# Optimization experiments

Measured on AMD Instinct MI355X. Metric: run time of the kernel, lower is better.

The kernel has to match this reference:

```python
import jax, jax.numpy as jnp
import numpy as np

B, D = 32768, 256          # batch, latent_size
L, K = 4, 2048             # n_codebooks, codebook_size
BETA = 0.25                # commitment loss weight (EMA layer uses only beta term)


def setup_inputs() -> dict:
    key = jax.random.key(0)
    kx, kc = jax.random.split(key)
    x = jax.random.normal(kx, (B, D), dtype=jnp.float32)
    # per-level codebooks (EMAVQLayer.embed, xavier-normal-ish scale)
    codebooks = jax.random.normal(kc, (L, K, D), dtype=jnp.float32) * 0.1
    return {"x": x, "codebooks": codebooks}


def reference(x, codebooks):
    """RQLayer.forward (EMA variant, eval-path math; EMA buffer updates are
    side effects and do not change forward outputs)."""
    sg = jax.lax.stop_gradient
    quantized = jnp.zeros_like(x)
    loss = jnp.zeros((), x.dtype)
    unused = jnp.zeros((), jnp.int32)
    inds = []
    for l in range(L):  # small fixed number of residual levels
        c = codebooks[l]                                   # [K, D]
        dist = (jnp.sum(x * x, axis=1, keepdims=True)
                - 2.0 * (x @ c.T)
                + jnp.sum(c * c, axis=1)[None, :])
        ind = jnp.argmin(dist, axis=1)                     # [B]
        x_q = c[ind]                                       # gather [B, D]
        counts = jnp.zeros((K,), jnp.int32).at[ind].add(1)
        unused = unused + jnp.sum(counts == 0)
        loss = loss + BETA * jnp.mean((x - sg(x_q)) ** 2)
        quant = x + sg(x_q - x)                            # straight-through
        x = x - quant                                      # residual (== sg(x - x_q))
        quantized = quantized + quant
        inds.append(ind)
    return quantized, loss / L, unused, jnp.stack(inds, axis=1)
```

## Files before the change

### kernel.cpp

```cpp
#include <hip/hip_runtime.h>

#define NT 512
#define B_ 32768
#define D_ 256
#define L_ 4
#define K_ 2048
#define BM 64
#define NBLK (B_/BM)
#define BETA_ 0.25f

#define OUT_LOSS   8388608
#define OUT_UNUSED 8388609
#define OUT_INDS   8388610


__global__ __launch_bounds__(256) void rq_prep(const float* __restrict__ cb,
                                               int* __restrict__ counts,
                                               float* __restrict__ cnorm) {
  int cw = blockIdx.x * 256 + threadIdx.x;
  if (cw >= L_ * K_) return;
  counts[cw] = 0;
  const float4* cb4 = (const float4*)cb;
  float s = 0.f;
  for (int d4 = 0; d4 < 64; ++d4) {
    float4 v = cb4[(size_t)cw * 64 + d4];
    s = __fadd_rn(s, __fmul_rn(v.x, v.x));
    s = __fadd_rn(s, __fmul_rn(v.y, v.y));
    s = __fadd_rn(s, __fmul_rn(v.z, v.z));
    s = __fadd_rn(s, __fmul_rn(v.w, v.w));
  }
  cnorm[cw] = s;
}

template<int CTRL>
__device__ __forceinline__ float dpp_f(float v) {
  return __int_as_float(__builtin_amdgcn_update_dpp(0, __float_as_int(v), CTRL, 0xF, 0xF, true));
}
template<int CTRL>
__device__ __forceinline__ int dpp_i(int v) {
  return __builtin_amdgcn_update_dpp(0, v, CTRL, 0xF, 0xF, true);
}
#define XOR1 0xB1
#define XOR2 0x4E

__global__ __attribute__((amdgpu_flat_work_group_size(NT, NT), amdgpu_waves_per_eu(1)))
void rq_main(
    const float* __restrict__ x, const float* __restrict__ cb,
    float* __restrict__ out, int* __restrict__ counts,
    const float* __restrict__ cnorm, float* __restrict__ lpart) {
  __shared__ float4 xs[64][65];
  __shared__ float4 cs[64][64];
  __shared__ float  red_v[8][64];
  __shared__ int    red_i[8][64];
  __shared__ float  xxs[64];
  __shared__ int    ind_s[64];
  __shared__ float  lred[NT];

  const int tid  = threadIdx.x;
  const int lane = tid & 63;
  const int wave = tid >> 6;
  const int dg   = lane & 3;
  const int p    = lane >> 2;
  const int row0 = blockIdx.x * BM;
  const float4* x4  = (const float4*)x;
  const float4* cb4 = (const float4*)cb;

  {
    float4 v[8];
    #pragma unroll
    for (int it = 0; it < 8; ++it)
      v[it] = x4[(size_t)(row0 + wave + (it << 3)) * 64 + lane];
    #pragma unroll
    for (int it = 0; it < 8; ++it)
      xs[wave + (it << 3)][lane] = v[it];
  }

  float4 st[8];
  #pragma unroll
  for (int it = 0; it < 8; ++it)
    st[it] = cb4[(size_t)(wave * 8 + it) * 64 + lane];
  #pragma unroll
  for (int it = 0; it < 8; ++it)
    cs[wave * 8 + it][lane] = st[it];

  const float4* xb = &xs[p * 4][dg];
  const float4* cvp[4];
  #pragma unroll
  for (int jj = 0; jj < 4; ++jj) cvp[jj] = &cs[wave * 8 + (jj ^ dg)][dg];

  float lsum = 0.f;
  const int kb = (wave << 3) | dg;
  float4* out4 = (float4*)out;

  for (int l = 0; l < L_; ++l) {
    __syncthreads();

    if (tid < 64) {
      float s = 0.f;
      for (int d4 = 0; d4 < 64; ++d4) {
        float4 v = xs[tid][d4];
        s = __fadd_rn(s, __fmul_rn(v.x, v.x));
        s = __fadd_rn(s, __fmul_rn(v.y, v.y));
        s = __fadd_rn(s, __fmul_rn(v.z, v.z));
        s = __fadd_rn(s, __fmul_rn(v.w, v.w));
      }
      xxs[tid] = s;
    }
    __syncthreads();

    float xxr[4];
    #pragma unroll
    for (int i = 0; i < 4; ++i) xxr[i] = xxs[p * 4 + i];

    float bv[4]; int bi[4];
    #pragma unroll
    for (int i = 0; i < 4; ++i) { bv[i] = 3.4e38f; bi[i] = 0; }
    const float* cnl = cnorm + l * K_;

    for (int ch = 0; ch < 32; ++ch) {
      {
        int tn = l * 32 + ch + 1; if (tn > 127) tn = 127;
        const float4* src = cb4 + (size_t)tn * 4096;
        #pragma unroll
        for (int it = 0; it < 8; ++it)
          st[it] = src[(size_t)(wave * 8 + it) * 64 + lane];
      }
      const float cn0 = cnl[(ch << 6) + kb];
      const float cn4 = cnl[(ch << 6) + kb + 4];

      float acc[4][8];

      {
        float4 xv[4], cv[8];
        #pragma unroll
        for (int i = 0; i < 4; ++i) xv[i] = xb[i * 65];
        #pragma unroll
        for (int j = 0; j < 4; ++j) { cv[j] = cvp[j][0]; cv[j + 4] = cvp[j][256]; }
        #pragma unroll
        for (int i = 0; i < 4; ++i)
          #pragma unroll
          for (int j = 0; j < 8; ++j) {
            float a = __fmul_rn(xv[i].x, cv[j].x);
            a = fmaf(xv[i].y, cv[j].y, a);
            a = fmaf(xv[i].z, cv[j].z, a);
            a = fmaf(xv[i].w, cv[j].w, a);
            acc[i][j] = a;
          }
      }
      #pragma unroll
      for (int t = 1; t < 16; ++t) {
        float4 xv[4], cv[8];
        #pragma unroll
        for (int i = 0; i < 4; ++i) xv[i] = xb[i * 65 + t * 4];
        #pragma unroll
        for (int j = 0; j < 4; ++j) { cv[j] = cvp[j][t * 4]; cv[j + 4] = cvp[j][t * 4 + 256]; }
        #pragma unroll
        for (int i = 0; i < 4; ++i)
          #pragma unroll
          for (int j = 0; j < 8; ++j) {
            acc[i][j] = fmaf(xv[i].x, cv[j].x, acc[i][j]);
            acc[i][j] = fmaf(xv[i].y, cv[j].y, acc[i][j]);
            acc[i][j] = fmaf(xv[i].z, cv[j].z, acc[i][j]);
            acc[i][j] = fmaf(xv[i].w, cv[j].w, acc[i][j]);
          }
      }

      #pragma unroll
      for (int it = 0; it < 8; ++it)
        cs[wave * 8 + it][lane] = st[it];

      #pragma unroll
      for (int i = 0; i < 4; ++i) {
        acc[i][0] += dpp_f<XOR1>(acc[i][1]);
        acc[i][2] += dpp_f<XOR1>(acc[i][3]);
        acc[i][0] += dpp_f<XOR2>(acc[i][2]);
        acc[i][4] += dpp_f<XOR1>(acc[i][5]);
        acc[i][6] += dpp_f<XOR1>(acc[i][7]);
        acc[i][4] += dpp_f<XOR2>(acc[i][6]);
      }

      const int kidx = (ch << 6) + kb;
      #pragma unroll
      for (int i = 0; i < 4; ++i) {
        float s0 = __fadd_rn(__fsub_rn(xxr[i], __fmul_rn(2.0f, acc[i][0])), cn0);
        if (s0 < bv[i]) { bv[i] = s0; bi[i] = kidx; }
        float s4 = __fadd_rn(__fsub_rn(xxr[i], __fmul_rn(2.0f, acc[i][4])), cn4);
        if (s4 < bv[i]) { bv[i] = s4; bi[i] = kidx + 4; }
      }
    }

    #pragma unroll
    for (int i = 0; i < 4; ++i) {
      { float pv = dpp_f<XOR1>(bv[i]); int pi = dpp_i<XOR1>(bi[i]);
        if (pv < bv[i] || (pv == bv[i] && pi < bi[i])) { bv[i] = pv; bi[i] = pi; } }
      { float pv = dpp_f<XOR2>(bv[i]); int pi = dpp_i<XOR2>(bi[i]);
        if (pv < bv[i] || (pv == bv[i] && pi < bi[i])) { bv[i] = pv; bi[i] = pi; } }
    }
    if (dg == 0) {
      #pragma unroll
      for (int i = 0; i < 4; ++i) {
        red_v[wave][p * 4 + i] = bv[i];
        red_i[wave][p * 4 + i] = bi[i];
      }
    }
    __syncthreads();
    if (tid < 64) {
      float bv_ = red_v[0][tid]; int bi_ = red_i[0][tid];
      #pragma unroll
      for (int w = 1; w < 8; ++w) {
        float v = red_v[w][tid]; int ii = red_i[w][tid];
        if (v < bv_ || (v == bv_ && ii < bi_)) { bv_ = v; bi_ = ii; }
      }
      ind_s[tid] = bi_;
      out[(size_t)OUT_INDS + (size_t)(row0 + tid) * L_ + l] = (float)bi_;
      atomicAdd(&counts[l * K_ + bi_], 1);
    }
    __syncthreads();

    #pragma unroll
    for (int it = 0; it < 8; ++it) {
      const int r = wave + (it << 3);
      const size_t oidx = (size_t)(row0 + r) * 64 + lane;
      float4 xv = xs[r][lane];
      float4 cv = cb4[(size_t)(l * K_ + ind_s[r]) * 64 + lane];
      float tx = __fsub_rn(cv.x, xv.x); float qx = __fadd_rn(xv.x, tx); float nx = __fsub_rn(xv.x, qx);
      float ty = __fsub_rn(cv.y, xv.y); float qy = __fadd_rn(xv.y, ty); float ny = __fsub_rn(xv.y, qy);
      float tz = __fsub_rn(cv.z, xv.z); float qz = __fadd_rn(xv.z, tz); float nz = __fsub_rn(xv.z, qz);
      float tw = __fsub_rn(cv.w, xv.w); float qw = __fadd_rn(xv.w, tw); float nw = __fsub_rn(xv.w, qw);
      float4 prev = (l == 0) ? make_float4(0.f, 0.f, 0.f, 0.f) : out4[oidx];
      out4[oidx] = make_float4(__fadd_rn(prev.x, qx), __fadd_rn(prev.y, qy),
                               __fadd_rn(prev.z, qz), __fadd_rn(prev.w, qw));
      float ex = __fsub_rn(xv.x, cv.x);
      float ey = __fsub_rn(xv.y, cv.y);
      float ez = __fsub_rn(xv.z, cv.z);
      float ew = __fsub_rn(xv.w, cv.w);
      lsum = __fadd_rn(lsum, __fmul_rn(ex, ex));
      lsum = __fadd_rn(lsum, __fmul_rn(ey, ey));
      lsum = __fadd_rn(lsum, __fmul_rn(ez, ez));
      lsum = __fadd_rn(lsum, __fmul_rn(ew, ew));
      xs[r][lane] = make_float4(nx, ny, nz, nw);
    }
  }

  lred[tid] = lsum;
  __syncthreads();
  for (int s = NT / 2; s > 0; s >>= 1) {
    if (tid < s) lred[tid] += lred[tid + s];
    __syncthreads();
  }
  if (tid == 0) lpart[blockIdx.x] = lred[0];
}

__global__ __launch_bounds__(256) void rq_final(const int* __restrict__ counts,
                                                const float* __restrict__ lpart,
                                                float* __restrict__ out) {
  __shared__ double fs[256];
  __shared__ int    is_[256];
  int tid = threadIdx.x;
  double ls = 0.0;
  for (int i = tid; i < NBLK; i += 256) ls += (double)lpart[i];
  int uz = 0;
  for (int i = tid; i < L_ * K_; i += 256) uz += (counts[i] == 0) ? 1 : 0;
  fs[tid] = ls; is_[tid] = uz;
  __syncthreads();
  for (int s = 128; s > 0; s >>= 1) {
    if (tid < s) { fs[tid] += fs[tid + s]; is_[tid] += is_[tid + s]; }
    __syncthreads();
  }
  if (tid == 0) {
    out[OUT_LOSS]   = (float)(fs[0] * (double)BETA_ / ((double)B_ * (double)D_ * (double)L_));
    out[OUT_UNUSED] = (float)is_[0];
  }
}

extern "C" void kernel_launch(void* const* d_in, const int* in_sizes, int n_in,
                              void* d_out, int out_size, void* d_ws, size_t ws_size,
                              hipStream_t stream) {
  const float* x  = (const float*)d_in[0];
  const float* cb = (const float*)d_in[1];
  float* out = (float*)d_out;
  int*   counts = (int*)d_ws;
  float* cnorm  = (float*)((char*)d_ws + 32768);
  float* lpart  = (float*)((char*)d_ws + 65536);

  rq_prep<<<(L_ * K_ + 255) / 256, 256, 0, stream>>>(cb, counts, cnorm);
  rq_main<<<NBLK, NT, 0, stream>>>(x, cb, out, counts, cnorm, lpart);
  rq_final<<<1, 256, 0, stream>>>(counts, lpart, out);
}
```

Measured before the change: 1.927 ms.

## Replace LDS-staged codebook tiles with wave-uniform scalar codebook loads

The distance loop is restructured so each lane owns one row and each wave handles 8 codewords per chunk. Codebook values are read straight from global memory at wave-uniform addresses, which the compiler can turn into scalar loads, instead of being staged through a double-buffered LDS tile. The x tile is transposed in LDS so the lane index is contiguous, and the DPP cross-lane reductions and the waves_per_eu(1) hint are dropped. This removes LDS traffic and staging for the codebook, but each thread now does 32 FMAs per float4 x load with less register blocking. It also depends on scalar-cache bandwidth for the codebook reads.

```diff
diff --git a/kernel.cpp b/kernel.cpp
--- a/kernel.cpp
+++ b/kernel.cpp
@@ -32,24 +32,12 @@
   cnorm[cw] = s;
 }
 
-template<int CTRL>
-__device__ __forceinline__ float dpp_f(float v) {
-  return __int_as_float(__builtin_amdgcn_update_dpp(0, __float_as_int(v), CTRL, 0xF, 0xF, true));
-}
-template<int CTRL>
-__device__ __forceinline__ int dpp_i(int v) {
-  return __builtin_amdgcn_update_dpp(0, v, CTRL, 0xF, 0xF, true);
-}
-#define XOR1 0xB1
-#define XOR2 0x4E
-
-__global__ __attribute__((amdgpu_flat_work_group_size(NT, NT), amdgpu_waves_per_eu(1)))
+__global__ __attribute__((amdgpu_flat_work_group_size(NT, NT)))
 void rq_main(
     const float* __restrict__ x, const float* __restrict__ cb,
     float* __restrict__ out, int* __restrict__ counts,
     const float* __restrict__ cnorm, float* __restrict__ lpart) {
-  __shared__ float4 xs[64][65];
-  __shared__ float4 cs[64][64];
+  __shared__ float4 xst[64][65];
   __shared__ float  red_v[8][64];
   __shared__ int    red_i[8][64];
   __shared__ float  xxs[64];
@@ -59,8 +47,7 @@
   const int tid  = threadIdx.x;
   const int lane = tid & 63;
   const int wave = tid >> 6;
-  const int dg   = lane & 3;
-  const int p    = lane >> 2;
+  const int wu   = __builtin_amdgcn_readfirstlane(wave);
   const int row0 = blockIdx.x * BM;
   const float4* x4  = (const float4*)x;
   const float4* cb4 = (const float4*)cb;
@@ -72,24 +59,10 @@
       v[it] = x4[(size_t)(row0 + wave + (it << 3)) * 64 + lane];
     #pragma unroll
     for (int it = 0; it < 8; ++it)
-      xs[wave + (it << 3)][lane] = v[it];
-  }
-
-  float4 st[8];
-  #pragma unroll
-  for (int it = 0; it < 8; ++it)
-    st[it] = cb4[(size_t)(wave * 8 + it) * 64 + lane];
-  #pragma unroll
-  for (int it = 0; it < 8; ++it)
-    cs[wave * 8 + it][lane] = st[it];
-
-  const float4* xb = &xs[p * 4][dg];
-  const float4* cvp[4];
-  #pragma unroll
-  for (int jj = 0; jj < 4; ++jj) cvp[jj] = &cs[wave * 8 + (jj ^ dg)][dg];
+      xst[lane][wave + (it << 3)] = v[it];
+  }
 
   float lsum = 0.f;
-  const int kb = (wave << 3) | dg;
   float4* out4 = (float4*)out;
 
   for (int l = 0; l < L_; ++l) {
@@ -98,7 +71,7 @@
     if (tid < 64) {
       float s = 0.f;
       for (int d4 = 0; d4 < 64; ++d4) {
-        float4 v = xs[tid][d4];
+        float4 v = xst[d4][tid];
         s = __fadd_rn(s, __fmul_rn(v.x, v.x));
         s = __fadd_rn(s, __fmul_rn(v.y, v.y));
         s = __fadd_rn(s, __fmul_rn(v.z, v.z));
@@ -108,101 +81,42 @@
     }
     __syncthreads();
 
-    float xxr[4];
-    #pragma unroll
-    for (int i = 0; i < 4; ++i) xxr[i] = xxs[p * 4 + i];
-
-    float bv[4]; int bi[4];
-    #pragma unroll
-    for (int i = 0; i < 4; ++i) { bv[i] = 3.4e38f; bi[i] = 0; }
+    const float xx = xxs[lane];
+    float bv = 3.4e38f; int bi = 0;
     const float* cnl = cnorm + l * K_;
+    const float* cwl = cb + ((size_t)l * K_ + (size_t)wu * 8) * 256;
 
     for (int ch = 0; ch < 32; ++ch) {
-      {
-        int tn = l * 32 + ch + 1; if (tn > 127) tn = 127;
-        const float4* src = cb4 + (size_t)tn * 4096;
+      const float* cwp = cwl + (size_t)ch * (64 * 256);
+
+      float acc[8];
+      #pragma unroll
+      for (int jj = 0; jj < 8; ++jj) acc[jj] = 0.f;
+
+      #pragma unroll 8
+      for (int t = 0; t < 64; ++t) {
+        const float4 xv = xst[t][lane];
         #pragma unroll
-        for (int it = 0; it < 8; ++it)
-          st[it] = src[(size_t)(wave * 8 + it) * 64 + lane];
-      }
-      const float cn0 = cnl[(ch << 6) + kb];
-      const float cn4 = cnl[(ch << 6) + kb + 4];
-
-      float acc[4][8];
-
-      {
-        float4 xv[4], cv[8];
-        #pragma unroll
-        for (int i = 0; i < 4; ++i) xv[i] = xb[i * 65];
-        #pragma unroll
-        for (int j = 0; j < 4; ++j) { cv[j] = cvp[j][0]; cv[j + 4] = cvp[j][256]; }
-        #pragma unroll
-        for (int i = 0; i < 4; ++i)
-          #pragma unroll
-          for (int j = 0; j < 8; ++j) {
-            float a = __fmul_rn(xv[i].x, cv[j].x);
-            a = fmaf(xv[i].y, cv[j].y, a);
-            a = fmaf(xv[i].z, cv[j].z, a);
-            a = fmaf(xv[i].w, cv[j].w, a);
-            acc[i][j] = a;
-          }
-      }
+        for (int jj = 0; jj < 8; ++jj) {
+          const float4 c = *(const float4*)(cwp + jj * 256 + t * 4);
+          acc[jj] = fmaf(xv.x, c.x, acc[jj]);
+          acc[jj] = fmaf(xv.y, c.y, acc[jj]);
+          acc[jj] = fmaf(xv.z, c.z, acc[jj]);
+          acc[jj] = fmaf(xv.w, c.w, acc[jj]);
+        }
+      }
+
+      const int kb0 = (ch << 6) + (wu << 3);
       #pragma unroll
-      for (int t = 1; t < 16; ++t) {
-        float4 xv[4], cv[8];
-        #pragma unroll
-        for (int i = 0; i < 4; ++i) xv[i] = xb[i * 65 + t * 4];
-        #pragma unroll
-        for (int j = 0; j < 4; ++j) { cv[j] = cvp[j][t * 4]; cv[j + 4] = cvp[j][t * 4 + 256]; }
-        #pragma unroll
-        for (int i = 0; i < 4; ++i)
-          #pragma unroll
-          for (int j = 0; j < 8; ++j) {
-            acc[i][j] = fmaf(xv[i].x, cv[j].x, acc[i][j]);
-            acc[i][j] = fmaf(xv[i].y, cv[j].y, acc[i][j]);
-            acc[i][j] = fmaf(xv[i].z, cv[j].z, acc[i][j]);
-            acc[i][j] = fmaf(xv[i].w, cv[j].w, acc[i][j]);
-          }
-      }
-
-      #pragma unroll
-      for (int it = 0; it < 8; ++it)
-        cs[wave * 8 + it][lane] = st[it];
-
-      #pragma unroll
-      for (int i = 0; i < 4; ++i) {
-        acc[i][0] += dpp_f<XOR1>(acc[i][1]);
-        acc[i][2] += dpp_f<XOR1>(acc[i][3]);
-        acc[i][0] += dpp_f<XOR2>(acc[i][2]);
-        acc[i][4] += dpp_f<XOR1>(acc[i][5]);
-        acc[i][6] += dpp_f<XOR1>(acc[i][7]);
-        acc[i][4] += dpp_f<XOR2>(acc[i][6]);
-      }
-
-      const int kidx = (ch << 6) + kb;
-      #pragma unroll
-      for (int i = 0; i < 4; ++i) {
-        float s0 = __fadd_rn(__fsub_rn(xxr[i], __fmul_rn(2.0f, acc[i][0])), cn0);
-        if (s0 < bv[i]) { bv[i] = s0; bi[i] = kidx; }
-        float s4 = __fadd_rn(__fsub_rn(xxr[i], __fmul_rn(2.0f, acc[i][4])), cn4);
-        if (s4 < bv[i]) { bv[i] = s4; bi[i] = kidx + 4; }
-      }
-    }
-
-    #pragma unroll
-    for (int i = 0; i < 4; ++i) {
-      { float pv = dpp_f<XOR1>(bv[i]); int pi = dpp_i<XOR1>(bi[i]);
-        if (pv < bv[i] || (pv == bv[i] && pi < bi[i])) { bv[i] = pv; bi[i] = pi; } }
-      { float pv = dpp_f<XOR2>(bv[i]); int pi = dpp_i<XOR2>(bi[i]);
-        if (pv < bv[i] || (pv == bv[i] && pi < bi[i])) { bv[i] = pv; bi[i] = pi; } }
-    }
-    if (dg == 0) {
-      #pragma unroll
-      for (int i = 0; i < 4; ++i) {
-        red_v[wave][p * 4 + i] = bv[i];
-        red_i[wave][p * 4 + i] = bi[i];
-      }
-    }
+      for (int jj = 0; jj < 8; ++jj) {
+        const float cn = cnl[kb0 + jj];
+        float s = __fadd_rn(__fsub_rn(xx, __fmul_rn(2.0f, acc[jj])), cn);
+        if (s < bv) { bv = s; bi = kb0 + jj; }
+      }
+    }
+
+    red_v[wave][lane] = bv;
+    red_i[wave][lane] = bi;
     __syncthreads();
     if (tid < 64) {
       float bv_ = red_v[0][tid]; int bi_ = red_i[0][tid];
@@ -221,7 +135,7 @@
     for (int it = 0; it < 8; ++it) {
       const int r = wave + (it << 3);
       const size_t oidx = (size_t)(row0 + r) * 64 + lane;
-      float4 xv = xs[r][lane];
+      float4 xv = xst[lane][r];
       float4 cv = cb4[(size_t)(l * K_ + ind_s[r]) * 64 + lane];
       float tx = __fsub_rn(cv.x, xv.x); float qx = __fadd_rn(xv.x, tx); float nx = __fsub_rn(xv.x, qx);
       float ty = __fsub_rn(cv.y, xv.y); float qy = __fadd_rn(xv.y, ty); float ny = __fsub_rn(xv.y, qy);
@@ -238,7 +152,7 @@
       lsum = __fadd_rn(lsum, __fmul_rn(ey, ey));
       lsum = __fadd_rn(lsum, __fmul_rn(ez, ez));
       lsum = __fadd_rn(lsum, __fmul_rn(ew, ew));
-      xs[r][lane] = make_float4(nx, ny, nz, nw);
+      xst[lane][r] = make_float4(nx, ny, nz, nw);
     }
   }
 
```

New measurement: 4.940 ms. 156% more time.
